# Kernel tuning notes

Measured on AMD Instinct MI355X. Metric: run time of the kernel, lower is better.

## Reference

```python
import jax, jax.numpy as jnp
import numpy as np

MARGIN = 1.0
N, D = 4096, 512
NUM_CLASSES = 64


def setup_inputs() -> dict:
    key = jax.random.key(0)
    k1, k2 = jax.random.split(key)
    inputs = jax.random.normal(k1, (N, D), dtype=jnp.float32)
    targets = jax.random.randint(k2, (N,), 0, NUM_CLASSES, dtype=jnp.int64)
    return {"inputs": inputs, "targets": targets}


def reference(inputs, targets):
    n = inputs.shape[0]
    sq = jnp.sum(inputs * inputs, axis=1)  # [n]
    # squared Euclidean distances, clamped at 0 (matches relu in original)
    d2 = jnp.maximum(sq[:, None] + sq[None, :] - 2.0 * (inputs @ inputs.T), 0.0)
    # safe sqrt (zero entries get 0, matching forward; avoids NaN grads)
    dist = jnp.where(d2 > 0, jnp.sqrt(jnp.where(d2 > 0, d2, 1.0)), 0.0)  # [n,n]

    same = targets[:, None] == targets[None, :]
    eye = jnp.eye(n, dtype=bool)
    pos_mask = same & ~eye          # positives, diagonal excluded
    neg_mask = ~same                # negatives (diagonal is same-label, excluded)

    # per-row sum_k exp(margin - d_ik) over negatives  (replaces per-pair loop)
    neg_sum = jnp.sum(jnp.where(neg_mask, jnp.exp(MARGIN - dist), 0.0), axis=1)  # [n]

    # J_ij = log(neg_sum_i + neg_sum_j) + d_ij for positive pairs
    J = jnp.log(neg_sum[:, None] + neg_sum[None, :]) + dist
    triu_pos = jnp.triu(pos_mask)   # loop iterated over upper-triangular positives
    hinge2 = jnp.where(triu_pos, jax.nn.relu(J) ** 2, 0.0)

    # original divides by count of ALL positive entries (both triangles)
    len_p = jnp.sum(pos_mask).astype(jnp.float32)
    return jnp.sum(hinge2) / len_p
```

## Files before the change

kernel.cpp:

```cpp
#include <hip/hip_runtime.h>
#include <math.h>

#define NN 4096
#define DD 512
#define MARGINF 1.0f
#define NCLS 64
#define MAXM 160
#define TRI (MAXM * (MAXM - 1) / 2)
#define NBLK 528

typedef __attribute__((ext_vector_type(8))) short bf16x8;
typedef __attribute__((ext_vector_type(4))) float f32x4;

#define WS_SQ   0
#define WS_NS   4096
#define WS_LOSS 8192
#define WS_CNT  8256
#define WS_RK   8320
#define WS_MEM  12416
#define WS_XB   32768
#define WS_PD   1081344

__device__ __forceinline__ unsigned short f2bf(float f) {
    unsigned u = __float_as_uint(f);
    u += 0x7fffu + ((u >> 16) & 1u);
    return (unsigned short)(u >> 16);
}

__global__ __launch_bounds__(256) void prep_kernel(const float* __restrict__ X,
                                                   float* __restrict__ ws) {
    const int wv = threadIdx.x >> 6, lane = threadIdx.x & 63;
    const int row = blockIdx.x * 4 + wv;
    const float4* xr = (const float4*)(X + (size_t)row * DD);
    float4 a = xr[lane], b = xr[lane + 64];
    float s = a.x * a.x + a.y * a.y + a.z * a.z + a.w * a.w
            + b.x * b.x + b.y * b.y + b.z * b.z + b.w * b.w;
#pragma unroll
    for (int off = 32; off; off >>= 1) s += __shfl_down(s, off, 64);
    if (lane == 0) { ws[WS_SQ + row] = s; ws[WS_NS + row] = 0.0f; }
    ushort4 pa = {f2bf(a.x), f2bf(a.y), f2bf(a.z), f2bf(a.w)};
    ushort4 pb = {f2bf(b.x), f2bf(b.y), f2bf(b.z), f2bf(b.w)};
    ushort4* xb = (ushort4*)((unsigned short*)(ws + WS_XB) + (size_t)row * DD);
    xb[lane] = pa;
    xb[lane + 64] = pb;
    if (blockIdx.x == 0) {
        if (threadIdx.x < NCLS) ((int*)(ws + WS_CNT))[threadIdx.x] = 0;
        if (threadIdx.x == 0) ws[WS_LOSS] = 0.0f;
    }
}

__global__ __launch_bounds__(256) void class_build_kernel(const int* __restrict__ tgt,
                                                          float* __restrict__ ws) {
    const int t = blockIdx.x * 256 + threadIdx.x;
    const int c = tgt[t];
    int p = atomicAdd(&((int*)(ws + WS_CNT))[c], 1);
    ((int*)(ws + WS_RK))[t] = p;
    if (p < MAXM) ((int*)(ws + WS_MEM))[c * MAXM + p] = t;
}

__global__ __launch_bounds__(256, 3) void negsum_kernel(const int* __restrict__ tgt,
                                                        float* __restrict__ ws) {
    __shared__ unsigned short As[128 * 32];
    __shared__ unsigned short Bs[128 * 32];

    const int bidx = blockIdx.x;
    int bj = (int)((sqrtf(8.0f * (float)bidx + 1.0f) - 1.0f) * 0.5f);
    while (bj * (bj + 1) / 2 > bidx) --bj;
    while ((bj + 1) * (bj + 2) / 2 <= bidx) ++bj;
    const int bi = bidx - bj * (bj + 1) / 2;
    const int i0 = bi * 128, j0 = bj * 128;

    const int tid = threadIdx.x;
    const int w = tid >> 6, lane = tid & 63;
    const unsigned short* Xb = (const unsigned short*)(ws + WS_XB);

    const int srow = tid >> 2, schk = tid & 3;
    const unsigned short* gA0 = Xb + (size_t)(i0 + srow) * DD + schk * 8;
    const unsigned short* gA1 = gA0 + (size_t)64 * DD;
    const unsigned short* gB0 = Xb + (size_t)(j0 + srow) * DD + schk * 8;
    const unsigned short* gB1 = gB0 + (size_t)64 * DD;

    const int m_ = lane & 15, q = lane >> 4;
    const int wr = (w & 1) * 64, wc = (w >> 1) * 64;

    f32x4 acc[4][4] = {};

    bf16x8 rA0 = *(const bf16x8*)gA0;
    bf16x8 rA1 = *(const bf16x8*)gA1;
    bf16x8 rB0 = *(const bf16x8*)gB0;
    bf16x8 rB1 = *(const bf16x8*)gB1;

    for (int it = 0; it < 16; ++it) {
        if (it) __syncthreads();
        *(bf16x8*)(As + tid * 8) = rA0;
        *(bf16x8*)(As + 2048 + tid * 8) = rA1;
        *(bf16x8*)(Bs + tid * 8) = rB0;
        *(bf16x8*)(Bs + 2048 + tid * 8) = rB1;
        if (it < 15) {
            rA0 = *(const bf16x8*)(gA0 + (it + 1) * 32);
            rA1 = *(const bf16x8*)(gA1 + (it + 1) * 32);
            rB0 = *(const bf16x8*)(gB0 + (it + 1) * 32);
            rB1 = *(const bf16x8*)(gB1 + (it + 1) * 32);
        }
        __syncthreads();
        bf16x8 af[4], bfr[4];
#pragma unroll
        for (int u = 0; u < 4; ++u)
            af[u] = *(const bf16x8*)(As + (wr + u * 16 + m_) * 32 + q * 8);
#pragma unroll
        for (int v = 0; v < 4; ++v)
            bfr[v] = *(const bf16x8*)(Bs + (wc + v * 16 + m_) * 32 + q * 8);
#pragma unroll
        for (int u = 0; u < 4; ++u)
#pragma unroll
            for (int v = 0; v < 4; ++v)
                acc[u][v] = __builtin_amdgcn_mfma_f32_16x16x32_bf16(
                    af[u], bfr[v], acc[u][v], 0, 0, 0);
    }

    const float* sq = ws + WS_SQ;
    float* ns = ws + WS_NS;
    const int* rk = (const int*)(ws + WS_RK);
    float* posd = ws + WS_PD;
    float sjv[4]; int tjv[4], jv[4];
#pragma unroll
    for (int v = 0; v < 4; ++v) {
        int j = j0 + wc + v * 16 + m_;
        jv[v] = j;
        sjv[v] = sq[j];
        tjv[v] = tgt[j];
    }
    float colp[4] = {0.0f, 0.0f, 0.0f, 0.0f};
#pragma unroll
    for (int u = 0; u < 4; ++u) {
#pragma unroll
        for (int r = 0; r < 4; ++r) {
            const int i = i0 + wr + u * 16 + q * 4 + r;
            const float si = sq[i];
            const int ti = tgt[i];
            float rp = 0.0f;
#pragma unroll
            for (int v = 0; v < 4; ++v) {
                float d2 = si + sjv[v] - 2.0f * acc[u][v][r];
                float dist = d2 > 0.0f ? sqrtf(d2) : 0.0f;
                if (tjv[v] != ti) {
                    float e = __expf(MARGINF - dist);
                    rp += e;
                    colp[v] += e;
                } else if (i < jv[v]) {
                    int ra = rk[i], rb = rk[jv[v]];
                    if (ra < MAXM && rb < MAXM) {
                        int hi = ra > rb ? ra : rb;
                        int lo = ra > rb ? rb : ra;
                        posd[ti * TRI + hi * (hi - 1) / 2 + lo] = dist;
                    }
                }
            }
            rp += __shfl_xor(rp, 1, 64);
            rp += __shfl_xor(rp, 2, 64);
            rp += __shfl_xor(rp, 4, 64);
            rp += __shfl_xor(rp, 8, 64);
            if (m_ == 0) atomicAdd(&ns[i], rp);
        }
    }
    if (bi != bj) {
#pragma unroll
        for (int v = 0; v < 4; ++v) {
            float cp = colp[v];
            cp += __shfl_xor(cp, 16, 64);
            cp += __shfl_xor(cp, 32, 64);
            if (q == 0) atomicAdd(&ns[jv[v]], cp);
        }
    }
}

__global__ __launch_bounds__(256) void pair2_kernel(float* __restrict__ ws) {
    __shared__ float wsum[4];
    const int c = blockIdx.x;
    int mc = ((const int*)(ws + WS_CNT))[c];
    if (mc > MAXM) mc = MAXM;
    const int P = mc * (mc - 1) / 2;
    const int* mem = (const int*)(ws + WS_MEM) + c * MAXM;
    const float* pd = ws + WS_PD + c * TRI;
    const float* ns = ws + WS_NS;
    float lsum = 0.0f;
    for (int p = threadIdx.x; p < P; p += 256) {
        int b = (int)((1.0f + sqrtf(1.0f + 8.0f * (float)p)) * 0.5f);
        while (b * (b - 1) / 2 > p) --b;
        while ((b + 1) * b / 2 <= p) ++b;
        const int a = p - b * (b - 1) / 2;
        const float dist = pd[b * (b - 1) / 2 + a];
        const int i = mem[a], j = mem[b];
        float J = __logf(ns[i] + ns[j]) + dist;
        float h = fmaxf(J, 0.0f);
        lsum += h * h;
    }
#pragma unroll
    for (int off = 32; off; off >>= 1) lsum += __shfl_xor(lsum, off, 64);
    const int wv = threadIdx.x >> 6, lane = threadIdx.x & 63;
    if (lane == 0) wsum[wv] = lsum;
    __syncthreads();
    if (threadIdx.x == 0) {
        float s = wsum[0] + wsum[1] + wsum[2] + wsum[3];
        if (s != 0.0f) atomicAdd(&ws[WS_LOSS], s);
    }
}

__global__ void finalize_kernel(const float* __restrict__ ws, float* __restrict__ out) {
    const int t = threadIdx.x;
    int mcv = (t < NCLS) ? ((const int*)(ws + WS_CNT))[t] : 0;
    float lp = (float)(mcv * (mcv - 1));
#pragma unroll
    for (int off = 32; off; off >>= 1) lp += __shfl_down(lp, off, 64);
    if (t == 0) out[0] = ws[WS_LOSS] / lp;
}

extern "C" void kernel_launch(void* const* d_in, const int* in_sizes, int n_in,
                              void* d_out, int out_size, void* d_ws, size_t ws_size,
                              hipStream_t stream) {
    const float* X  = (const float*)d_in[0];
    const int*  tgt = (const int*)d_in[1];
    float* ws  = (float*)d_ws;
    float* out = (float*)d_out;

    hipLaunchKernelGGL(prep_kernel, dim3(NN / 4), dim3(256), 0, stream, X, ws);
    hipLaunchKernelGGL(class_build_kernel, dim3(NN / 256), dim3(256), 0, stream, tgt, ws);
    hipLaunchKernelGGL(negsum_kernel, dim3(NBLK), dim3(256), 0, stream, tgt, ws);
    hipLaunchKernelGGL(pair2_kernel, dim3(NCLS), dim3(256), 0, stream, ws);
    hipLaunchKernelGGL(finalize_kernel, dim3(1), dim3(64), 0, stream, ws, out);
}
```

Baseline: 122.6 us.

## Store bf16 inputs in MFMA fragment layout and fuse finalize into pair kernel

The prep kernel now writes the bf16 copy of the inputs directly in the per-lane MFMA fragment order. This lets the Gram-tile kernel load its A/B fragments straight from global memory with register double-buffering instead of staging through LDS with two barriers per k-step. Separately, the finalize kernel is folded into the pair kernel using a last-block atomic counter, removing one launch. The cost is heavier global/L2 traffic per wave, since the shared-memory reuse is gone, and a fence-based completion pattern.

Result: no change. 124.5 us (+1.6%).

```diff
diff --git a/kernel.cpp b/kernel.cpp
--- a/kernel.cpp
+++ b/kernel.cpp
@@ -15,10 +15,11 @@
 #define WS_SQ   0
 #define WS_NS   4096
 #define WS_LOSS 8192
+#define WS_CTR  8193
 #define WS_CNT  8256
 #define WS_RK   8320
 #define WS_MEM  12416
-#define WS_XB   32768
+#define WS_XF   32768
 #define WS_PD   1081344
 
 __device__ __forceinline__ unsigned short f2bf(float f) {
@@ -32,7 +33,7 @@
     const int wv = threadIdx.x >> 6, lane = threadIdx.x & 63;
     const int row = blockIdx.x * 4 + wv;
     const float4* xr = (const float4*)(X + (size_t)row * DD);
-    float4 a = xr[lane], b = xr[lane + 64];
+    float4 a = xr[2 * lane], b = xr[2 * lane + 1];
     float s = a.x * a.x + a.y * a.y + a.z * a.z + a.w * a.w
             + b.x * b.x + b.y * b.y + b.z * b.z + b.w * b.w;
 #pragma unroll
@@ -40,12 +41,15 @@
     if (lane == 0) { ws[WS_SQ + row] = s; ws[WS_NS + row] = 0.0f; }
     ushort4 pa = {f2bf(a.x), f2bf(a.y), f2bf(a.z), f2bf(a.w)};
     ushort4 pb = {f2bf(b.x), f2bf(b.y), f2bf(b.z), f2bf(b.w)};
-    ushort4* xb = (ushort4*)((unsigned short*)(ws + WS_XB) + (size_t)row * DD);
-    xb[lane] = pa;
-    xb[lane + 64] = pb;
+    const int r16 = row >> 4, m = row & 15;
+    const int kb = lane >> 2, q = lane & 3;
+    ushort4* dst = (ushort4*)((unsigned short*)(ws + WS_XF)
+                              + ((size_t)(r16 * 16 + kb) * 64 + q * 16 + m) * 8);
+    dst[0] = pa;
+    dst[1] = pb;
     if (blockIdx.x == 0) {
         if (threadIdx.x < NCLS) ((int*)(ws + WS_CNT))[threadIdx.x] = 0;
-        if (threadIdx.x == 0) ws[WS_LOSS] = 0.0f;
+        if (threadIdx.x == 0) { ws[WS_LOSS] = 0.0f; ((unsigned*)ws)[WS_CTR] = 0u; }
     }
 }
 
@@ -60,9 +64,6 @@
 
 __global__ __launch_bounds__(256, 3) void negsum_kernel(const int* __restrict__ tgt,
                                                         float* __restrict__ ws) {
-    __shared__ unsigned short As[128 * 32];
-    __shared__ unsigned short Bs[128 * 32];
-
     const int bidx = blockIdx.x;
     int bj = (int)((sqrtf(8.0f * (float)bidx + 1.0f) - 1.0f) * 0.5f);
     while (bj * (bj + 1) / 2 > bidx) --bj;
@@ -72,50 +73,39 @@
 
     const int tid = threadIdx.x;
     const int w = tid >> 6, lane = tid & 63;
-    const unsigned short* Xb = (const unsigned short*)(ws + WS_XB);
-
-    const int srow = tid >> 2, schk = tid & 3;
-    const unsigned short* gA0 = Xb + (size_t)(i0 + srow) * DD + schk * 8;
-    const unsigned short* gA1 = gA0 + (size_t)64 * DD;
-    const unsigned short* gB0 = Xb + (size_t)(j0 + srow) * DD + schk * 8;
-    const unsigned short* gB1 = gB0 + (size_t)64 * DD;
-
     const int m_ = lane & 15, q = lane >> 4;
     const int wr = (w & 1) * 64, wc = (w >> 1) * 64;
+    const unsigned short* Xf = (const unsigned short*)(ws + WS_XF);
+
+    const int air = (i0 + wr) >> 4;
+    const int bjr = (j0 + wc) >> 4;
+    const unsigned short* pA = Xf + (size_t)air * 16 * 512 + lane * 8;
+    const unsigned short* pB = Xf + (size_t)bjr * 16 * 512 + lane * 8;
 
     f32x4 acc[4][4] = {};
-
-    bf16x8 rA0 = *(const bf16x8*)gA0;
-    bf16x8 rA1 = *(const bf16x8*)gA1;
-    bf16x8 rB0 = *(const bf16x8*)gB0;
-    bf16x8 rB1 = *(const bf16x8*)gB1;
-
+    bf16x8 af[4], bfr[4], nA[4], nB[4];
+#pragma unroll
+    for (int u = 0; u < 4; ++u) {
+        af[u]  = *(const bf16x8*)(pA + (size_t)u * 16 * 512);
+        bfr[u] = *(const bf16x8*)(pB + (size_t)u * 16 * 512);
+    }
+#pragma unroll
     for (int it = 0; it < 16; ++it) {
-        if (it) __syncthreads();
-        *(bf16x8*)(As + tid * 8) = rA0;
-        *(bf16x8*)(As + 2048 + tid * 8) = rA1;
-        *(bf16x8*)(Bs + tid * 8) = rB0;
-        *(bf16x8*)(Bs + 2048 + tid * 8) = rB1;
         if (it < 15) {
-            rA0 = *(const bf16x8*)(gA0 + (it + 1) * 32);
-            rA1 = *(const bf16x8*)(gA1 + (it + 1) * 32);
-            rB0 = *(const bf16x8*)(gB0 + (it + 1) * 32);
-            rB1 = *(const bf16x8*)(gB1 + (it + 1) * 32);
-        }
-        __syncthreads();
-        bf16x8 af[4], bfr[4];
-#pragma unroll
-        for (int u = 0; u < 4; ++u)
-            af[u] = *(const bf16x8*)(As + (wr + u * 16 + m_) * 32 + q * 8);
-#pragma unroll
-        for (int v = 0; v < 4; ++v)
-            bfr[v] = *(const bf16x8*)(Bs + (wc + v * 16 + m_) * 32 + q * 8);
+#pragma unroll
+            for (int u = 0; u < 4; ++u) {
+                nA[u] = *(const bf16x8*)(pA + (size_t)u * 16 * 512 + (it + 1) * 512);
+                nB[u] = *(const bf16x8*)(pB + (size_t)u * 16 * 512 + (it + 1) * 512);
+            }
+        }
 #pragma unroll
         for (int u = 0; u < 4; ++u)
 #pragma unroll
             for (int v = 0; v < 4; ++v)
                 acc[u][v] = __builtin_amdgcn_mfma_f32_16x16x32_bf16(
                     af[u], bfr[v], acc[u][v], 0, 0, 0);
+#pragma unroll
+        for (int u = 0; u < 4; ++u) { af[u] = nA[u]; bfr[u] = nB[u]; }
     }
 
     const float* sq = ws + WS_SQ;
@@ -174,9 +164,12 @@
     }
 }
 
-__global__ __launch_bounds__(256) void pair2_kernel(float* __restrict__ ws) {
+__global__ __launch_bounds__(256) void pair2_kernel(float* __restrict__ ws,
+                                                    float* __restrict__ out) {
     __shared__ float wsum[4];
+    __shared__ bool last;
     const int c = blockIdx.x;
+    const int tid = threadIdx.x;
     int mc = ((const int*)(ws + WS_CNT))[c];
     if (mc > MAXM) mc = MAXM;
     const int P = mc * (mc - 1) / 2;
@@ -184,7 +177,7 @@
     const float* pd = ws + WS_PD + c * TRI;
     const float* ns = ws + WS_NS;
     float lsum = 0.0f;
-    for (int p = threadIdx.x; p < P; p += 256) {
+    for (int p = tid; p < P; p += 256) {
         int b = (int)((1.0f + sqrtf(1.0f + 8.0f * (float)p)) * 0.5f);
         while (b * (b - 1) / 2 > p) --b;
         while ((b + 1) * b / 2 <= p) ++b;
@@ -197,22 +190,27 @@
     }
 #pragma unroll
     for (int off = 32; off; off >>= 1) lsum += __shfl_xor(lsum, off, 64);
-    const int wv = threadIdx.x >> 6, lane = threadIdx.x & 63;
+    const int wv = tid >> 6, lane = tid & 63;
     if (lane == 0) wsum[wv] = lsum;
     __syncthreads();
-    if (threadIdx.x == 0) {
+    if (tid == 0) {
         float s = wsum[0] + wsum[1] + wsum[2] + wsum[3];
         if (s != 0.0f) atomicAdd(&ws[WS_LOSS], s);
-    }
-}
-
-__global__ void finalize_kernel(const float* __restrict__ ws, float* __restrict__ out) {
-    const int t = threadIdx.x;
-    int mcv = (t < NCLS) ? ((const int*)(ws + WS_CNT))[t] : 0;
-    float lp = (float)(mcv * (mcv - 1));
-#pragma unroll
-    for (int off = 32; off; off >>= 1) lp += __shfl_down(lp, off, 64);
-    if (t == 0) out[0] = ws[WS_LOSS] / lp;
+        __threadfence();
+        unsigned d = atomicAdd((unsigned*)ws + WS_CTR, 1u);
+        last = (d == NCLS - 1);
+    }
+    __syncthreads();
+    if (last && tid < 64) {
+        int mcv = ((const int*)(ws + WS_CNT))[tid];
+        float lp = (float)(mcv * (mcv - 1));
+#pragma unroll
+        for (int off = 32; off; off >>= 1) lp += __shfl_down(lp, off, 64);
+        if (tid == 0) {
+            float total = atomicAdd(&ws[WS_LOSS], 0.0f);
+            out[0] = total / lp;
+        }
+    }
 }
 
 extern "C" void kernel_launch(void* const* d_in, const int* in_sizes, int n_in,
@@ -226,6 +224,5 @@
     hipLaunchKernelGGL(prep_kernel, dim3(NN / 4), dim3(256), 0, stream, X, ws);
     hipLaunchKernelGGL(class_build_kernel, dim3(NN / 256), dim3(256), 0, stream, tgt, ws);
     hipLaunchKernelGGL(negsum_kernel, dim3(NBLK), dim3(256), 0, stream, tgt, ws);
-    hipLaunchKernelGGL(pair2_kernel, dim3(NCLS), dim3(256), 0, stream, ws);
-    hipLaunchKernelGGL(finalize_kernel, dim3(1), dim3(64), 0, stream, ws, out);
-}
+    hipLaunchKernelGGL(pair2_kernel, dim3(NCLS), dim3(256), 0, stream, ws, out);
+}
```
